# Kernel optimization log

Hardware: AMD Instinct MI355X
Metric: run time of the kernel (lower is better)

## Reference

```python
import jax, jax.numpy as jnp
import numpy as np

RADIUS, HMIN, HMAX, NSAMPLE = 0.05, -0.02, 0.04, 32
EPS = 1e-5


def setup_inputs() -> dict:
    key = jax.random.key(0)
    ks = jax.random.split(key, 6)
    B, N, C, OUT = 4, 2048, 256, 256
    seed_xyz_graspable = jax.random.uniform(ks[0], (B, N, 3), jnp.float32) * 0.2
    seed_features_graspable = jax.random.normal(ks[1], (B, C, N), jnp.float32)
    vp_rot = jax.random.normal(ks[2], (B, N, 3, 3), jnp.float32)
    W1 = jax.random.normal(ks[3], (OUT, 3 + C), jnp.float32) * 0.02
    W2 = jax.random.normal(ks[4], (OUT, OUT), jnp.float32) * 0.02
    return {
        "seed_xyz_graspable": seed_xyz_graspable,
        "seed_features_graspable": seed_features_graspable,
        "vp_rot": vp_rot,
        "W1": W1, "gamma1": jnp.ones((OUT,), jnp.float32), "beta1": jnp.zeros((OUT,), jnp.float32),
        "W2": W2, "gamma2": jnp.ones((OUT,), jnp.float32), "beta2": jnp.zeros((OUT,), jnp.float32),
    }


def _cylinder_query(xyz, rot):
    # xyz: (B,N,3), rot: (B,N,3,3); new_xyz == xyz.
    B, N, _ = xyz.shape
    d = xyz[:, None, :, :] - xyz[:, :, None, :]                  # (B,P,N,3) offsets to each candidate
    r = jnp.einsum('bpij,bpnj->bpni', rot, d)                    # rotate into cylinder frame (rot @ d)
    mask = (r[..., 1] ** 2 + r[..., 2] ** 2 < RADIUS ** 2) & (r[..., 0] > HMIN) & (r[..., 0] < HMAX)
    order = jnp.arange(N, dtype=jnp.int32)
    keys = jnp.where(mask, order, order + N)                     # in-cylinder points sort first, stable order
    _, idx = jax.lax.top_k(-keys, NSAMPLE)                       # first NSAMPLE indices satisfying the query
    valid = jnp.take_along_axis(mask, idx, axis=-1)
    first = idx[..., :1]
    any_valid = valid[..., :1]
    idx = jnp.where(valid, idx, jnp.where(any_valid, first, 0))  # pad with first hit like the CUDA kernel
    return idx                                                   # (B,P,NSAMPLE) int32


def _group(xyz, features, rot, idx):
    gxyz = jax.vmap(lambda a, i: a[i])(xyz, idx)                 # (B,P,S,3)
    gxyz = (gxyz - xyz[:, :, None, :]) / RADIUS                  # center on query + normalize_xyz
    gxyz = jnp.einsum('bpsj,bpjk->bpsk', gxyz, rot)              # rotate_xyz: grouped_xyz @ rot
    gfeat = jax.vmap(lambda f, i: f[:, i])(features, idx)        # (B,C,P,S)
    return jnp.concatenate([gxyz.transpose(0, 3, 1, 2), gfeat], axis=1)  # (B,3+C,P,S)


def _conv_bn_relu(x, W, gamma, beta):
    y = jnp.einsum('oc,bcps->bops', W, x)                        # 1x1 conv, no bias (bn=True)
    mu = y.mean(axis=(0, 2, 3), keepdims=True)
    var = y.var(axis=(0, 2, 3), keepdims=True)
    y = (y - mu) * jax.lax.rsqrt(var + EPS)
    y = y * gamma[None, :, None, None] + beta[None, :, None, None]
    return jax.nn.relu(y)


def reference(seed_xyz_graspable, seed_features_graspable, vp_rot, W1, gamma1, beta1, W2, gamma2, beta2):
    idx = _cylinder_query(seed_xyz_graspable, vp_rot)
    g = _group(seed_xyz_graspable, seed_features_graspable, vp_rot, idx)
    h = _conv_bn_relu(g, W1, gamma1, beta1)
    h = _conv_bn_relu(h, W2, gamma2, beta2)
    return h.max(axis=3)                                         # maxpool over nsample -> (B,OUT,P)
```

## Files before the change

kernel.cpp:

```cpp
#include <hip/hip_runtime.h>

typedef unsigned short u16;
typedef unsigned int u32;
typedef __attribute__((ext_vector_type(8))) short bf16x8;
typedef __attribute__((ext_vector_type(4))) float f32x4;

#define NPTS 2048
#define CFEAT 256
#define NS 32
#define MTOT 262144
#define NBLK 4096
#define INV_N (1.0f/262144.0f)

__device__ __forceinline__ float bf2f(u16 u) {
    union { u32 i; float f; } v; v.i = ((u32)u) << 16; return v.f;
}
__device__ __forceinline__ u16 f2bf(float f) {
    union { float f; u32 i; } v; v.f = f;
    u32 i = v.i;
    return (u16)((i + 0x7fffu + ((i >> 16) & 1u)) >> 16);
}

__device__ __forceinline__ void gload16(const void* g, void* l) {
    __builtin_amdgcn_global_load_lds((const __attribute__((address_space(1))) void*)g,
                                     (__attribute__((address_space(3))) void*)l, 16, 0, 0);
}

__global__ __launch_bounds__(256) void prep_k(const float* __restrict__ W1, const float* __restrict__ W2,
                                              u16* __restrict__ Wp1, u16* __restrict__ Wp2) {
    int o = blockIdx.x, t = threadIdx.x;
    Wp1[o * 288 + t] = f2bf(W1[o * 259 + 3 + t]);
    if (t < 32) Wp1[o * 288 + 256 + t] = (t < 3) ? f2bf(W1[o * 259 + t]) : (u16)0;
    Wp2[o * 256 + t] = f2bf(W2[o * 256 + t]);
}

__global__ __launch_bounds__(256) void query_k(const float* __restrict__ xyz, const float* __restrict__ rot,
                                               int* __restrict__ idx) {
    int pid = blockIdx.x * 4 + (threadIdx.x >> 6);
    int lane = threadIdx.x & 63;
    int b = pid >> 11, p = pid & 2047;
    const float* xb = xyz + (size_t)b * NPTS * 3;
    float px = xb[p * 3 + 0], py = xb[p * 3 + 1], pz = xb[p * 3 + 2];
    const float* rp = rot + (size_t)pid * 9;
    float r00 = rp[0], r01 = rp[1], r02 = rp[2];
    float r10 = rp[3], r11 = rp[4], r12 = rp[5];
    float r20 = rp[6], r21 = rp[7], r22 = rp[8];
    int cnt = 0, first = 0;
    for (int n0 = 0; n0 < NPTS && cnt < NS; n0 += 64) {
        int n = n0 + lane;
        float dx = __fsub_rn(xb[n * 3 + 0], px);
        float dy = __fsub_rn(xb[n * 3 + 1], py);
        float dz = __fsub_rn(xb[n * 3 + 2], pz);
        float a0 = __fadd_rn(__fadd_rn(__fmul_rn(r00, dx), __fmul_rn(r01, dy)), __fmul_rn(r02, dz));
        float a1 = __fadd_rn(__fadd_rn(__fmul_rn(r10, dx), __fmul_rn(r11, dy)), __fmul_rn(r12, dz));
        float a2 = __fadd_rn(__fadd_rn(__fmul_rn(r20, dx), __fmul_rn(r21, dy)), __fmul_rn(r22, dz));
        float t2 = __fadd_rn(__fmul_rn(a1, a1), __fmul_rn(a2, a2));
        bool valid = (t2 < 0.0025f) && (a0 > -0.02f) && (a0 < 0.04f);
        unsigned long long bal = __ballot(valid);
        if (cnt == 0 && bal) first = n0 + __builtin_ctzll(bal);
        int rank = __builtin_popcountll(bal & ((1ull << lane) - 1ull));
        int slot = cnt + rank;
        if (valid && slot < NS) idx[(size_t)pid * NS + slot] = n;
        cnt += __builtin_popcountll(bal);
    }
    int filled = cnt < NS ? cnt : NS;
    if (lane >= filled && lane < NS) idx[(size_t)pid * NS + lane] = (cnt > 0) ? first : 0;
}

__global__ __launch_bounds__(256) void featT_k(const float* __restrict__ feat, u16* __restrict__ featT) {
    __shared__ float sm[32 * 33];
    int b = blockIdx.z;
    int n0 = blockIdx.x * 32, c0 = blockIdx.y * 32;
    int t = threadIdx.x, x = t & 31, y = t >> 5;
    #pragma unroll
    for (int rr = 0; rr < 4; rr++) {
        int c = c0 + y + rr * 8;
        sm[(y + rr * 8) * 33 + x] = feat[((size_t)(b * CFEAT + c)) * NPTS + n0 + x];
    }
    __syncthreads();
    #pragma unroll
    for (int rr = 0; rr < 4; rr++) {
        int n = n0 + y + rr * 8;
        featT[((size_t)(b * NPTS + n)) * CFEAT + c0 + x] = f2bf(sm[x * 33 + (y + rr * 8)]);
    }
}

__global__ __launch_bounds__(256) void gxyz_k(const float* __restrict__ xyz, const float* __restrict__ rot,
                                              const int* __restrict__ idx, u16* __restrict__ gxyz) {
    int m = blockIdx.x * 256 + threadIdx.x;
    int pid = m >> 5;
    int b = pid >> 11, p = pid & 2047;
    int i = idx[m];
    const float* xb = xyz + (size_t)b * NPTS * 3;
    float dx = (xb[i * 3 + 0] - xb[p * 3 + 0]) * 20.0f;
    float dy = (xb[i * 3 + 1] - xb[p * 3 + 1]) * 20.0f;
    float dz = (xb[i * 3 + 2] - xb[p * 3 + 2]) * 20.0f;
    const float* rp = rot + (size_t)pid * 9;
    float g0 = dx * rp[0] + dy * rp[3] + dz * rp[6];
    float g1 = dx * rp[1] + dy * rp[4] + dz * rp[7];
    float g2 = dx * rp[2] + dy * rp[5] + dz * rp[8];
    uint2 v;
    v.x = (u32)f2bf(g0) | ((u32)f2bf(g1) << 16);
    v.y = (u32)f2bf(g2);
    *(uint2*)(gxyz + (size_t)m * 4) = v;
}

template <int FULL, int STORE>
__global__ __launch_bounds__(256) void fused_k(
    const u16* __restrict__ featT, const u16* __restrict__ gxyz, const int* __restrict__ idx,
    const u16* __restrict__ Wp1, const u16* __restrict__ Wp2, const float* __restrict__ ab1,
    float* __restrict__ psum, float* __restrict__ psq,
    float* __restrict__ ymax, float* __restrict__ ymin, uint2* __restrict__ y1f)
{
    __shared__ __attribute__((aligned(16))) u16 As[64 * 32];
    __shared__ __attribute__((aligned(16))) u16 Bs[256 * 32];
    __shared__ __attribute__((aligned(16))) u16 y1s[FULL ? 64 * 264 : 16];
    __shared__ int rowbase_s[64];

    const int tid = threadIdx.x;
    const int lane = tid & 63, wave = tid >> 6;
    const int quad = lane >> 4, tl = lane & 15;
    const int bx = blockIdx.x;
    const int m0 = bx * 64;

    if (tid < 64) {
        int m = m0 + tid;
        int gi = idx[m];
        int b = m >> 16;
        rowbase_s[tid] = (b * NPTS + gi) * CFEAT;
    }
    __syncthreads();
    const int srow = tid >> 2, sc16 = tid & 3;
    const int abase = rowbase_s[srow] + sc16 * 8;

    f32x4 acc[4][4];
    #pragma unroll
    for (int i = 0; i < 4; i++)
        #pragma unroll
        for (int j = 0; j < 4; j++) acc[i][j] = (f32x4){0.f, 0.f, 0.f, 0.f};

    auto mfma_tile = [&](f32x4 (&ac)[4][4], const u16* a_lds, int a_stride) {
        bf16x8 af[4], bv[4];
        #pragma unroll
        for (int i = 0; i < 4; i++) af[i] = *(const bf16x8*)(a_lds + (i * 16 + tl) * a_stride + quad * 8);
        #pragma unroll
        for (int j = 0; j < 4; j++) bv[j] = *(const bf16x8*)(Bs + (wave * 64 + j * 16 + tl) * 32 + quad * 8);
        #pragma unroll
        for (int i = 0; i < 4; i++)
            #pragma unroll
            for (int j = 0; j < 4; j++)
                ac[i][j] = __builtin_amdgcn_mfma_f32_16x16x32_bf16(af[i], bv[j], ac[i][j], 0, 0, 0);
    };

    for (int ks = 0; ks < 8; ks++) {
        const int k0 = ks * 32;
        __syncthreads();
        gload16(featT + abase + k0, As + tid * 8);
        #pragma unroll
        for (int q = 0; q < 4; q++)
            gload16(Wp1 + (srow + q * 64) * 288 + k0 + sc16 * 8, Bs + q * 2048 + tid * 8);
        __syncthreads();
        mfma_tile(acc, As, 32);
    }
    {
        __syncthreads();
        uint4 va = make_uint4(0, 0, 0, 0);
        if (sc16 == 0) {
            uint2 g2 = *(const uint2*)(gxyz + (size_t)(m0 + srow) * 4);
            va.x = g2.x; va.y = g2.y;
        }
        *(uint4*)(As + srow * 32 + sc16 * 8) = va;
        #pragma unroll
        for (int q = 0; q < 4; q++)
            gload16(Wp1 + (srow + q * 64) * 288 + 256 + sc16 * 8, Bs + q * 2048 + tid * 8);
        __syncthreads();
        mfma_tile(acc, As, 32);
    }

    if (!FULL) {
        #pragma unroll
        for (int j = 0; j < 4; j++) {
            float s = 0.f, q2 = 0.f;
            #pragma unroll
            for (int i = 0; i < 4; i++) {
                float v0 = acc[i][j][0], v1 = acc[i][j][1], v2 = acc[i][j][2], v3 = acc[i][j][3];
                if (STORE) {
                    u32 lo = (u32)f2bf(v0) | ((u32)f2bf(v1) << 16);
                    u32 hi = (u32)f2bf(v2) | ((u32)f2bf(v3) << 16);
                    y1f[((size_t)(bx * 4 + wave) * 16 + i * 4 + j) * 64 + lane] = make_uint2(lo, hi);
                    v0 = bf2f((u16)(lo & 0xffff)); v1 = bf2f((u16)(lo >> 16));
                    v2 = bf2f((u16)(hi & 0xffff)); v3 = bf2f((u16)(hi >> 16));
                }
                s += v0 + v1 + v2 + v3;
                q2 += v0 * v0 + v1 * v1 + v2 * v2 + v3 * v3;
            }
            s += __shfl_xor(s, 16); s += __shfl_xor(s, 32);
            q2 += __shfl_xor(q2, 16); q2 += __shfl_xor(q2, 32);
            if (quad == 0) {
                int col = wave * 64 + j * 16 + tl;
                psum[(size_t)bx * 256 + col] = s;
                psq[(size_t)bx * 256 + col] = q2;
            }
        }
        return;
    }

    #pragma unroll
    for (int j = 0; j < 4; j++) {
        int col = wave * 64 + j * 16 + tl;
        float a = ab1[col], bb = ab1[256 + col];
        #pragma unroll
        for (int i = 0; i < 4; i++)
            #pragma unroll
            for (int r = 0; r < 4; r++) {
                float v = fmaxf(fmaf(acc[i][j][r], a, bb), 0.f);
                y1s[(i * 16 + quad * 4 + r) * 264 + col] = f2bf(v);
            }
    }

    f32x4 acc2[4][4];
    #pragma unroll
    for (int i = 0; i < 4; i++)
        #pragma unroll
        for (int j = 0; j < 4; j++) acc2[i][j] = (f32x4){0.f, 0.f, 0.f, 0.f};
    for (int ks = 0; ks < 8; ks++) {
        const int k0 = ks * 32;
        __syncthreads();
        #pragma unroll
        for (int q = 0; q < 4; q++)
            gload16(Wp2 + (srow + q * 64) * 256 + k0 + sc16 * 8, Bs + q * 2048 + tid * 8);
        __syncthreads();
        mfma_tile(acc2, y1s + k0, 264);
    }

    #pragma unroll
    for (int j = 0; j < 4; j++) {
        int col = wave * 64 + j * 16 + tl;
        float s = 0.f, q2 = 0.f;
        float mx0 = -3.0e38f, mn0 = 3.0e38f, mx1 = -3.0e38f, mn1 = 3.0e38f;
        #pragma unroll
        for (int i = 0; i < 4; i++)
            #pragma unroll
            for (int r = 0; r < 4; r++) {
                float v = acc2[i][j][r];
                s += v; q2 += v * v;
                if (i < 2) { mx0 = fmaxf(mx0, v); mn0 = fminf(mn0, v); }
                else       { mx1 = fmaxf(mx1, v); mn1 = fminf(mn1, v); }
            }
        s += __shfl_xor(s, 16); s += __shfl_xor(s, 32);
        q2 += __shfl_xor(q2, 16); q2 += __shfl_xor(q2, 32);
        mx0 = fmaxf(mx0, __shfl_xor(mx0, 16)); mx0 = fmaxf(mx0, __shfl_xor(mx0, 32));
        mn0 = fminf(mn0, __shfl_xor(mn0, 16)); mn0 = fminf(mn0, __shfl_xor(mn0, 32));
        mx1 = fmaxf(mx1, __shfl_xor(mx1, 16)); mx1 = fmaxf(mx1, __shfl_xor(mx1, 32));
        mn1 = fminf(mn1, __shfl_xor(mn1, 16)); mn1 = fminf(mn1, __shfl_xor(mn1, 32));
        if (quad == 0) {
            psum[(size_t)bx * 256 + col] = s;
            psq[(size_t)bx * 256 + col] = q2;
            size_t p0 = (size_t)(bx * 2) * 256 + col;
            size_t p1 = (size_t)(bx * 2 + 1) * 256 + col;
            ymax[p0] = mx0; ymin[p0] = mn0;
            ymax[p1] = mx1; ymin[p1] = mn1;
        }
    }
}

__global__ __launch_bounds__(256) void fused2_k(
    const uint2* __restrict__ y1f, const u16* __restrict__ Wp2, const float* __restrict__ ab1,
    float* __restrict__ psum, float* __restrict__ psq,
    float* __restrict__ ymax, float* __restrict__ ymin)
{
    __shared__ __attribute__((aligned(16))) u16 Bs[256 * 32];
    __shared__ __attribute__((aligned(16))) u16 y1s[64 * 264];
    const int tid = threadIdx.x;
    const int lane = tid & 63, wave = tid >> 6;
    const int quad = lane >> 4, tl = lane & 15;
    const int bx = blockIdx.x;

    #pragma unroll
    for (int j = 0; j < 4; j++) {
        int col = wave * 64 + j * 16 + tl;
        float a = ab1[col], bb = ab1[256 + col];
        #pragma unroll
        for (int i = 0; i < 4; i++) {
            uint2 v = y1f[((size_t)(bx * 4 + wave) * 16 + i * 4 + j) * 64 + lane];
            float f0 = bf2f((u16)(v.x & 0xffff)), f1 = bf2f((u16)(v.x >> 16));
            float f2 = bf2f((u16)(v.y & 0xffff)), f3 = bf2f((u16)(v.y >> 16));
            int rb = (i * 16 + quad * 4) * 264 + col;
            y1s[rb] = f2bf(fmaxf(fmaf(f0, a, bb), 0.f));
            y1s[rb + 264] = f2bf(fmaxf(fmaf(f1, a, bb), 0.f));
            y1s[rb + 528] = f2bf(fmaxf(fmaf(f2, a, bb), 0.f));
            y1s[rb + 792] = f2bf(fmaxf(fmaf(f3, a, bb), 0.f));
        }
    }

    const int srow = tid >> 2, sc16 = tid & 3;
    f32x4 acc2[4][4];
    #pragma unroll
    for (int i = 0; i < 4; i++)
        #pragma unroll
        for (int j = 0; j < 4; j++) acc2[i][j] = (f32x4){0.f, 0.f, 0.f, 0.f};

    for (int ks = 0; ks < 8; ks++) {
        const int k0 = ks * 32;
        __syncthreads();
        #pragma unroll
        for (int q = 0; q < 4; q++)
            gload16(Wp2 + (srow + q * 64) * 256 + k0 + sc16 * 8, Bs + q * 2048 + tid * 8);
        __syncthreads();
        bf16x8 af[4], bv[4];
        #pragma unroll
        for (int i = 0; i < 4; i++) af[i] = *(const bf16x8*)(y1s + (i * 16 + tl) * 264 + k0 + quad * 8);
        #pragma unroll
        for (int j = 0; j < 4; j++) bv[j] = *(const bf16x8*)(Bs + (wave * 64 + j * 16 + tl) * 32 + quad * 8);
        #pragma unroll
        for (int i = 0; i < 4; i++)
            #pragma unroll
            for (int j = 0; j < 4; j++)
                acc2[i][j] = __builtin_amdgcn_mfma_f32_16x16x32_bf16(af[i], bv[j], acc2[i][j], 0, 0, 0);
    }

    #pragma unroll
    for (int j = 0; j < 4; j++) {
        int col = wave * 64 + j * 16 + tl;
        float s = 0.f, q2 = 0.f;
        float mx0 = -3.0e38f, mn0 = 3.0e38f, mx1 = -3.0e38f, mn1 = 3.0e38f;
        #pragma unroll
        for (int i = 0; i < 4; i++)
            #pragma unroll
            for (int r = 0; r < 4; r++) {
                float v = acc2[i][j][r];
                s += v; q2 += v * v;
                if (i < 2) { mx0 = fmaxf(mx0, v); mn0 = fminf(mn0, v); }
                else       { mx1 = fmaxf(mx1, v); mn1 = fminf(mn1, v); }
            }
        s += __shfl_xor(s, 16); s += __shfl_xor(s, 32);
        q2 += __shfl_xor(q2, 16); q2 += __shfl_xor(q2, 32);
        mx0 = fmaxf(mx0, __shfl_xor(mx0, 16)); mx0 = fmaxf(mx0, __shfl_xor(mx0, 32));
        mn0 = fminf(mn0, __shfl_xor(mn0, 16)); mn0 = fminf(mn0, __shfl_xor(mn0, 32));
        mx1 = fmaxf(mx1, __shfl_xor(mx1, 16)); mx1 = fmaxf(mx1, __shfl_xor(mx1, 32));
        mn1 = fminf(mn1, __shfl_xor(mn1, 16)); mn1 = fminf(mn1, __shfl_xor(mn1, 32));
        if (quad == 0) {
            psum[(size_t)bx * 256 + col] = s;
            psq[(size_t)bx * 256 + col] = q2;
            size_t p0 = (size_t)(bx * 2) * 256 + col;
            size_t p1 = (size_t)(bx * 2 + 1) * 256 + col;
            ymax[p0] = mx0; ymin[p0] = mn0;
            ymax[p1] = mx1; ymin[p1] = mn1;
        }
    }
}

__global__ __launch_bounds__(256) void reduce1_k(const float* __restrict__ psum, const float* __restrict__ psq,
                                                 float* __restrict__ ps2, float* __restrict__ pq2) {
    int j = blockIdx.x, t = threadIdx.x;
    float s = 0.f, q = 0.f;
    #pragma unroll 4
    for (int kk = 0; kk < 16; kk++) {
        size_t r = (size_t)(j * 16 + kk) * 256 + t;
        s += psum[r]; q += psq[r];
    }
    ps2[j * 256 + t] = s;
    pq2[j * 256 + t] = q;
}

__global__ __launch_bounds__(256) void reduce2_k(const float* __restrict__ ps2, const float* __restrict__ pq2,
                                                 const float* __restrict__ gamma, const float* __restrict__ beta,
                                                 float* __restrict__ ab) {
    int c = threadIdx.x;
    float S = 0.f, Q = 0.f;
    for (int j = 0; j < 256; j++) {
        S += ps2[j * 256 + c];
        Q += pq2[j * 256 + c];
    }
    float mu = S * INV_N;
    float var = Q * INV_N - mu * mu;
    float a = gamma[c] * rsqrtf(var + 1e-5f);
    ab[c] = a;
    ab[256 + c] = beta[c] - mu * a;
}

__global__ __launch_bounds__(256) void final_k(const float* __restrict__ ymax, const float* __restrict__ ymin,
                                               const float* __restrict__ ab, float* __restrict__ out) {
    __shared__ float sm[32 * 33];
    int b = blockIdx.z;
    int n0 = blockIdx.x * 32, o0 = blockIdx.y * 32;
    int t = threadIdx.x, x = t & 31, y = t >> 5;
    #pragma unroll
    for (int rr = 0; rr < 4; rr++) {
        int n = n0 + y + rr * 8;
        int o = o0 + x;
        float a = ab[o], bb = ab[256 + o];
        size_t p = (size_t)(b * NPTS + n) * 256 + o;
        float v = (a >= 0.f) ? ymax[p] : ymin[p];
        sm[(y + rr * 8) * 33 + x] = fmaxf(fmaf(v, a, bb), 0.f);
    }
    __syncthreads();
    #pragma unroll
    for (int rr = 0; rr < 4; rr++)
        out[((size_t)(b * 256 + o0 + y + rr * 8)) * NPTS + n0 + x] = sm[x * 33 + (y + rr * 8)];
}

extern "C" void kernel_launch(void* const* d_in, const int* in_sizes, int n_in,
                              void* d_out, int out_size, void* d_ws, size_t ws_size,
                              hipStream_t stream) {
    const float* xyz    = (const float*)d_in[0];
    const float* feat   = (const float*)d_in[1];
    const float* rot    = (const float*)d_in[2];
    const float* W1     = (const float*)d_in[3];
    const float* gamma1 = (const float*)d_in[4];
    const float* beta1  = (const float*)d_in[5];
    const float* W2     = (const float*)d_in[6];
    const float* gamma2 = (const float*)d_in[7];
    const float* beta2  = (const float*)d_in[8];
    float* out = (float*)d_out;

    char* ws = (char*)d_ws;
    u16*   featT = (u16*)(ws + 0);
    int*   idx   = (int*)(ws + 4194304);
    u16*   gxyz  = (u16*)(ws + 5242880);
    u16*   Wp1   = (u16*)(ws + 7340032);
    u16*   Wp2   = (u16*)(ws + 7487488);
    float* ab1   = (float*)(ws + 7618560);
    float* ab2   = (float*)(ws + 7620608);
    float* psum  = (float*)(ws + 7622656);
    float* psq   = (float*)(ws + 11816960);
    float* ymax  = (float*)(ws + 16011264);
    float* ymin  = (float*)(ws + 24399872);
    uint2* y1f   = (uint2*)(ws + 32788480);
    const size_t BIG_NEED = 32788480ull + 134217728ull;

    float* r1s = (float*)(ws + 24399872);
    float* r1q = r1s + 65536;
    float* r2s = (float*)(ws + 5242880);
    float* r2q = r2s + 65536;

    prep_k<<<256, 256, 0, stream>>>(W1, W2, Wp1, Wp2);
    query_k<<<2048, 256, 0, stream>>>(xyz, rot, idx);
    featT_k<<<dim3(64, 8, 4), 256, 0, stream>>>(feat, featT);
    gxyz_k<<<1024, 256, 0, stream>>>(xyz, rot, idx, gxyz);

    if (ws_size >= BIG_NEED) {
        fused_k<0, 1><<<NBLK, 256, 0, stream>>>(featT, gxyz, idx, Wp1, Wp2, ab1, psum, psq, ymax, ymin, y1f);
        reduce1_k<<<256, 256, 0, stream>>>(psum, psq, r1s, r1q);
        reduce2_k<<<1, 256, 0, stream>>>(r1s, r1q, gamma1, beta1, ab1);
        fused2_k<<<NBLK, 256, 0, stream>>>(y1f, Wp2, ab1, psum, psq, ymax, ymin);
        reduce1_k<<<256, 256, 0, stream>>>(psum, psq, r2s, r2q);
        reduce2_k<<<1, 256, 0, stream>>>(r2s, r2q, gamma2, beta2, ab2);
    } else {
        fused_k<0, 0><<<NBLK, 256, 0, stream>>>(featT, gxyz, idx, Wp1, Wp2, ab1, psum, psq, ymax, ymin, nullptr);
        reduce1_k<<<256, 256, 0, stream>>>(psum, psq, r1s, r1q);
        reduce2_k<<<1, 256, 0, stream>>>(r1s, r1q, gamma1, beta1, ab1);
        fused_k<1, 0><<<NBLK, 256, 0, stream>>>(featT, gxyz, idx, Wp1, Wp2, ab1, psum, psq, ymax, ymin, nullptr);
        reduce1_k<<<256, 256, 0, stream>>>(psum, psq, r2s, r2q);
        reduce2_k<<<1, 256, 0, stream>>>(r2s, r2q, gamma2, beta2, ab2);
    }
    final_k<<<dim3(64, 8, 4), 256, 0, stream>>>(ymax, ymin, ab2, out);
}
```

Before: 258.2 us.

## Compute BN1 statistics from per-point GEMM weighted by gather counts

Layer-1 batch-norm statistics are no longer computed over the full gathered 262144-row GEMM. They come from a GEMM over only the 8192 unique points, weighted by how often each point is gathered, plus closed-form terms for the xyz channels (counts via atomics, second moments of gxyz). This removes the separate first-pass GEMM and the large bf16 intermediate buffer. The full kernel also double-buffers its LDS tiles to overlap global loads with MFMA. The trade-offs are atomic contention in count_k and a small change in numerics, since statistics now come from fp32 accumulators rather than bf16-rounded values.

```diff
diff --git a/kernel.cpp b/kernel.cpp
--- a/kernel.cpp
+++ b/kernel.cpp
@@ -10,6 +10,7 @@
 #define NS 32
 #define MTOT 262144
 #define NBLK 4096
+#define NROW 8192
 #define INV_N (1.0f/262144.0f)
 
 __device__ __forceinline__ float bf2f(u16 u) {
@@ -105,16 +106,141 @@
     *(uint2*)(gxyz + (size_t)m * 4) = v;
 }
 
-template <int FULL, int STORE>
-__global__ __launch_bounds__(256) void fused_k(
+__global__ __launch_bounds__(256) void zero_k(float* __restrict__ p, int n) {
+    int i = blockIdx.x * 256 + threadIdx.x;
+    if (i < n) p[i] = 0.f;
+}
+
+__global__ __launch_bounds__(256) void count_k(const int* __restrict__ idx, const u16* __restrict__ gxyz,
+                                               float* __restrict__ cntx, float* __restrict__ xstat) {
+    __shared__ float red[9 * 4];
+    int t = threadIdx.x, lane = t & 63, wave = t >> 6;
+    float p[9] = {0.f,0.f,0.f,0.f,0.f,0.f,0.f,0.f,0.f};
+    #pragma unroll
+    for (int u = 0; u < 4; u++) {
+        int m = blockIdx.x * 1024 + u * 256 + t;
+        int b = m >> 16;
+        int r = (b << 11) + idx[m];
+        uint2 v = *(const uint2*)(gxyz + (size_t)m * 4);
+        float x0 = bf2f((u16)(v.x & 0xffff));
+        float x1 = bf2f((u16)(v.x >> 16));
+        float x2 = bf2f((u16)(v.y & 0xffff));
+        atomicAdd(cntx + r * 4 + 0, 1.f);
+        atomicAdd(cntx + r * 4 + 1, x0);
+        atomicAdd(cntx + r * 4 + 2, x1);
+        atomicAdd(cntx + r * 4 + 3, x2);
+        p[0] += x0; p[1] += x1; p[2] += x2;
+        p[3] += x0 * x0; p[4] += x0 * x1; p[5] += x0 * x2;
+        p[6] += x1 * x1; p[7] += x1 * x2; p[8] += x2 * x2;
+    }
+    #pragma unroll
+    for (int k = 0; k < 9; k++) {
+        float s = p[k];
+        #pragma unroll
+        for (int o = 1; o < 64; o <<= 1) s += __shfl_xor(s, o);
+        if (lane == 0) red[k * 4 + wave] = s;
+    }
+    __syncthreads();
+    if (t < 9) atomicAdd(xstat + t, red[t * 4 + 0] + red[t * 4 + 1] + red[t * 4 + 2] + red[t * 4 + 3]);
+}
+
+__global__ __launch_bounds__(256) void zgemm_k(const u16* __restrict__ featT, const u16* __restrict__ Wp1,
+                                               const float* __restrict__ cntx,
+                                               float* __restrict__ Sacc, float* __restrict__ Qacc,
+                                               float* __restrict__ Xacc) {
+    __shared__ __attribute__((aligned(16))) u16 As[64 * 32];
+    __shared__ __attribute__((aligned(16))) u16 Bs[256 * 32];
+    const int tid = threadIdx.x;
+    const int lane = tid & 63, wave = tid >> 6;
+    const int quad = lane >> 4, tl = lane & 15;
+    const int m0 = blockIdx.x * 64;
+    const int srow = tid >> 2, sc16 = tid & 3;
+    const int abase = (m0 + srow) * CFEAT + sc16 * 8;
+
+    f32x4 acc[4][4];
+    #pragma unroll
+    for (int i = 0; i < 4; i++)
+        #pragma unroll
+        for (int j = 0; j < 4; j++) acc[i][j] = (f32x4){0.f, 0.f, 0.f, 0.f};
+
+    for (int ks = 0; ks < 8; ks++) {
+        const int k0 = ks * 32;
+        __syncthreads();
+        gload16(featT + abase + k0, As + tid * 8);
+        #pragma unroll
+        for (int q = 0; q < 4; q++)
+            gload16(Wp1 + (srow + q * 64) * 288 + k0 + sc16 * 8, Bs + q * 2048 + tid * 8);
+        __syncthreads();
+        bf16x8 af[4], bv[4];
+        #pragma unroll
+        for (int i = 0; i < 4; i++) af[i] = *(const bf16x8*)(As + (i * 16 + tl) * 32 + quad * 8);
+        #pragma unroll
+        for (int j = 0; j < 4; j++) bv[j] = *(const bf16x8*)(Bs + (wave * 64 + j * 16 + tl) * 32 + quad * 8);
+        #pragma unroll
+        for (int i = 0; i < 4; i++)
+            #pragma unroll
+            for (int j = 0; j < 4; j++)
+                acc[i][j] = __builtin_amdgcn_mfma_f32_16x16x32_bf16(af[i], bv[j], acc[i][j], 0, 0, 0);
+    }
+
+    #pragma unroll
+    for (int j = 0; j < 4; j++) {
+        int col = wave * 64 + j * 16 + tl;
+        float wx0 = bf2f(Wp1[col * 288 + 256]);
+        float wx1 = bf2f(Wp1[col * 288 + 257]);
+        float wx2 = bf2f(Wp1[col * 288 + 258]);
+        float S = 0.f, Q = 0.f, X = 0.f;
+        #pragma unroll
+        for (int i = 0; i < 4; i++)
+            #pragma unroll
+            for (int rr = 0; rr < 4; rr++) {
+                int row = i * 16 + quad * 4 + rr;
+                float4 cx = *(const float4*)(cntx + (size_t)(m0 + row) * 4);
+                float z = acc[i][j][rr];
+                S += cx.x * z;
+                Q += cx.x * z * z;
+                X += z * (wx0 * cx.y + wx1 * cx.z + wx2 * cx.w);
+            }
+        S += __shfl_xor(S, 16); S += __shfl_xor(S, 32);
+        Q += __shfl_xor(Q, 16); Q += __shfl_xor(Q, 32);
+        X += __shfl_xor(X, 16); X += __shfl_xor(X, 32);
+        if (quad == 0) {
+            atomicAdd(Sacc + col, S);
+            atomicAdd(Qacc + col, Q);
+            atomicAdd(Xacc + col, X);
+        }
+    }
+}
+
+__global__ __launch_bounds__(256) void ab1_k(const float* __restrict__ Sacc, const float* __restrict__ Qacc,
+                                             const float* __restrict__ Xacc, const float* __restrict__ xstat,
+                                             const u16* __restrict__ Wp1,
+                                             const float* __restrict__ gamma, const float* __restrict__ beta,
+                                             float* __restrict__ ab) {
+    int c = threadIdx.x;
+    float wx0 = bf2f(Wp1[c * 288 + 256]);
+    float wx1 = bf2f(Wp1[c * 288 + 257]);
+    float wx2 = bf2f(Wp1[c * 288 + 258]);
+    float S = Sacc[c] + wx0 * xstat[0] + wx1 * xstat[1] + wx2 * xstat[2];
+    float qxx = wx0 * wx0 * xstat[3] + wx1 * wx1 * xstat[6] + wx2 * wx2 * xstat[8]
+              + 2.f * (wx0 * wx1 * xstat[4] + wx0 * wx2 * xstat[5] + wx1 * wx2 * xstat[7]);
+    float Q = Qacc[c] + 2.f * Xacc[c] + qxx;
+    float mu = S * INV_N;
+    float var = Q * INV_N - mu * mu;
+    float a = gamma[c] * rsqrtf(var + 1e-5f);
+    ab[c] = a;
+    ab[256 + c] = beta[c] - mu * a;
+}
+
+__global__ __launch_bounds__(256) void full_k(
     const u16* __restrict__ featT, const u16* __restrict__ gxyz, const int* __restrict__ idx,
     const u16* __restrict__ Wp1, const u16* __restrict__ Wp2, const float* __restrict__ ab1,
     float* __restrict__ psum, float* __restrict__ psq,
-    float* __restrict__ ymax, float* __restrict__ ymin, uint2* __restrict__ y1f)
+    float* __restrict__ ymax, float* __restrict__ ymin)
 {
-    __shared__ __attribute__((aligned(16))) u16 As[64 * 32];
-    __shared__ __attribute__((aligned(16))) u16 Bs[256 * 32];
-    __shared__ __attribute__((aligned(16))) u16 y1s[FULL ? 64 * 264 : 16];
+    __shared__ __attribute__((aligned(16))) u16 As[2][64 * 32];
+    __shared__ __attribute__((aligned(16))) u16 Bs[2][256 * 32];
+    __shared__ __attribute__((aligned(16))) u16 y1s[64 * 264];
     __shared__ int rowbase_s[64];
 
     const int tid = threadIdx.x;
@@ -133,18 +259,12 @@
     const int srow = tid >> 2, sc16 = tid & 3;
     const int abase = rowbase_s[srow] + sc16 * 8;
 
-    f32x4 acc[4][4];
-    #pragma unroll
-    for (int i = 0; i < 4; i++)
-        #pragma unroll
-        for (int j = 0; j < 4; j++) acc[i][j] = (f32x4){0.f, 0.f, 0.f, 0.f};
-
-    auto mfma_tile = [&](f32x4 (&ac)[4][4], const u16* a_lds, int a_stride) {
+    auto mfma_tile = [&](f32x4 (&ac)[4][4], const u16* a_lds, int a_stride, const u16* b_lds) {
         bf16x8 af[4], bv[4];
         #pragma unroll
         for (int i = 0; i < 4; i++) af[i] = *(const bf16x8*)(a_lds + (i * 16 + tl) * a_stride + quad * 8);
         #pragma unroll
-        for (int j = 0; j < 4; j++) bv[j] = *(const bf16x8*)(Bs + (wave * 64 + j * 16 + tl) * 32 + quad * 8);
+        for (int j = 0; j < 4; j++) bv[j] = *(const bf16x8*)(b_lds + (wave * 64 + j * 16 + tl) * 32 + quad * 8);
         #pragma unroll
         for (int i = 0; i < 4; i++)
             #pragma unroll
@@ -152,57 +272,38 @@
                 ac[i][j] = __builtin_amdgcn_mfma_f32_16x16x32_bf16(af[i], bv[j], ac[i][j], 0, 0, 0);
     };
 
-    for (int ks = 0; ks < 8; ks++) {
-        const int k0 = ks * 32;
-        __syncthreads();
-        gload16(featT + abase + k0, As + tid * 8);
-        #pragma unroll
-        for (int q = 0; q < 4; q++)
-            gload16(Wp1 + (srow + q * 64) * 288 + k0 + sc16 * 8, Bs + q * 2048 + tid * 8);
-        __syncthreads();
-        mfma_tile(acc, As, 32);
-    }
-    {
-        __syncthreads();
-        uint4 va = make_uint4(0, 0, 0, 0);
-        if (sc16 == 0) {
-            uint2 g2 = *(const uint2*)(gxyz + (size_t)(m0 + srow) * 4);
-            va.x = g2.x; va.y = g2.y;
+    auto stage1 = [&](int t, int buf) {
+        if (t < 8) {
+            gload16(featT + abase + t * 32, &As[buf][tid * 8]);
+            #pragma unroll
+            for (int q = 0; q < 4; q++)
+                gload16(Wp1 + (srow + q * 64) * 288 + t * 32 + sc16 * 8, &Bs[buf][q * 2048 + tid * 8]);
+        } else {
+            uint4 va = make_uint4(0, 0, 0, 0);
+            if (sc16 == 0) {
+                uint2 g2 = *(const uint2*)(gxyz + (size_t)(m0 + srow) * 4);
+                va.x = g2.x; va.y = g2.y;
+            }
+            *(uint4*)(&As[buf][srow * 32 + sc16 * 8]) = va;
+            #pragma unroll
+            for (int q = 0; q < 4; q++)
+                gload16(Wp1 + (srow + q * 64) * 288 + 256 + sc16 * 8, &Bs[buf][q * 2048 + tid * 8]);
         }
-        *(uint4*)(As + srow * 32 + sc16 * 8) = va;
-        #pragma unroll
-        for (int q = 0; q < 4; q++)
-            gload16(Wp1 + (srow + q * 64) * 288 + 256 + sc16 * 8, Bs + q * 2048 + tid * 8);
-        __syncthreads();
-        mfma_tile(acc, As, 32);
-    }
-
-    if (!FULL) {
-        #pragma unroll
-        for (int j = 0; j < 4; j++) {
-            float s = 0.f, q2 = 0.f;
-            #pragma unroll
-            for (int i = 0; i < 4; i++) {
-                float v0 = acc[i][j][0], v1 = acc[i][j][1], v2 = acc[i][j][2], v3 = acc[i][j][3];
-                if (STORE) {
-                    u32 lo = (u32)f2bf(v0) | ((u32)f2bf(v1) << 16);
-                    u32 hi = (u32)f2bf(v2) | ((u32)f2bf(v3) << 16);
-                    y1f[((size_t)(bx * 4 + wave) * 16 + i * 4 + j) * 64 + lane] = make_uint2(lo, hi);
-                    v0 = bf2f((u16)(lo & 0xffff)); v1 = bf2f((u16)(lo >> 16));
-                    v2 = bf2f((u16)(hi & 0xffff)); v3 = bf2f((u16)(hi >> 16));
-                }
-                s += v0 + v1 + v2 + v3;
-                q2 += v0 * v0 + v1 * v1 + v2 * v2 + v3 * v3;
-            }
-            s += __shfl_xor(s, 16); s += __shfl_xor(s, 32);
-            q2 += __shfl_xor(q2, 16); q2 += __shfl_xor(q2, 32);
-            if (quad == 0) {
-                int col = wave * 64 + j * 16 + tl;
-                psum[(size_t)bx * 256 + col] = s;
-                psq[(size_t)bx * 256 + col] = q2;
-            }
-        }
-        return;
+    };
+
+    f32x4 acc[4][4];
+    #pragma unroll
+    for (int i = 0; i < 4; i++)
+        #pragma unroll
+        for (int j = 0; j < 4; j++) acc[i][j] = (f32x4){0.f, 0.f, 0.f, 0.f};
+
+    stage1(0, 0);
+    __syncthreads();
+    for (int t = 0; t < 9; t++) {
+        const int cur = t & 1;
+        if (t < 8) stage1(t + 1, cur ^ 1);
+        mfma_tile(acc, &As[cur][0], 32, &Bs[cur][0]);
+        __syncthreads();
     }
 
     #pragma unroll
@@ -217,20 +318,25 @@
                 y1s[(i * 16 + quad * 4 + r) * 264 + col] = f2bf(v);
             }
     }
+    #pragma unroll
+    for (int q = 0; q < 4; q++)
+        gload16(Wp2 + (srow + q * 64) * 256 + sc16 * 8, &Bs[0][q * 2048 + tid * 8]);
+    __syncthreads();
 
     f32x4 acc2[4][4];
     #pragma unroll
     for (int i = 0; i < 4; i++)
         #pragma unroll
         for (int j = 0; j < 4; j++) acc2[i][j] = (f32x4){0.f, 0.f, 0.f, 0.f};
-    for (int ks = 0; ks < 8; ks++) {
-        const int k0 = ks * 32;
-        __syncthreads();
-        #pragma unroll
-        for (int q = 0; q < 4; q++)
-            gload16(Wp2 + (srow + q * 64) * 256 + k0 + sc16 * 8, Bs + q * 2048 + tid * 8);
-        __syncthreads();
-        mfma_tile(acc2, y1s + k0, 264);
+    for (int t = 0; t < 8; t++) {
+        const int cur = t & 1;
+        if (t < 7) {
+            #pragma unroll
+            for (int q = 0; q < 4; q++)
+                gload16(Wp2 + (srow + q * 64) * 256 + (t + 1) * 32 + sc16 * 8, &Bs[cur ^ 1][q * 2048 + tid * 8]);
+        }
+        mfma_tile(acc2, y1s + t * 32, 264, &Bs[cur][0]);
+        __syncthreads();
     }
 
     #pragma unroll
@@ -264,42 +370,117 @@
     }
 }
 
-__global__ __launch_bounds__(256) void fused2_k(
-    const uint2* __restrict__ y1f, const u16* __restrict__ Wp2, const float* __restrict__ ab1,
+template <int FULL>
+__global__ __launch_bounds__(256) void fused_k(
+    const u16* __restrict__ featT, const u16* __restrict__ gxyz, const int* __restrict__ idx,
+    const u16* __restrict__ Wp1, const u16* __restrict__ Wp2, const float* __restrict__ ab1,
     float* __restrict__ psum, float* __restrict__ psq,
     float* __restrict__ ymax, float* __restrict__ ymin)
 {
+    __shared__ __attribute__((aligned(16))) u16 As[64 * 32];
     __shared__ __attribute__((aligned(16))) u16 Bs[256 * 32];
-    __shared__ __attribute__((aligned(16))) u16 y1s[64 * 264];
+    __shared__ __attribute__((aligned(16))) u16 y1s[FULL ? 64 * 264 : 16];
+    __shared__ int rowbase_s[64];
+
     const int tid = threadIdx.x;
     const int lane = tid & 63, wave = tid >> 6;
     const int quad = lane >> 4, tl = lane & 15;
     const int bx = blockIdx.x;
+    const int m0 = bx * 64;
+
+    if (tid < 64) {
+        int m = m0 + tid;
+        int gi = idx[m];
+        int b = m >> 16;
+        rowbase_s[tid] = (b * NPTS + gi) * CFEAT;
+    }
+    __syncthreads();
+    const int srow = tid >> 2, sc16 = tid & 3;
+    const int abase = rowbase_s[srow] + sc16 * 8;
+
+    f32x4 acc[4][4];
+    #pragma unroll
+    for (int i = 0; i < 4; i++)
+        #pragma unroll
+        for (int j = 0; j < 4; j++) acc[i][j] = (f32x4){0.f, 0.f, 0.f, 0.f};
+
+    auto mfma_tile = [&](f32x4 (&ac)[4][4], const u16* a_lds, int a_stride) {
+        bf16x8 af[4], bv[4];
+        #pragma unroll
+        for (int i = 0; i < 4; i++) af[i] = *(const bf16x8*)(a_lds + (i * 16 + tl) * a_stride + quad * 8);
+        #pragma unroll
+        for (int j = 0; j < 4; j++) bv[j] = *(const bf16x8*)(Bs + (wave * 64 + j * 16 + tl) * 32 + quad * 8);
+        #pragma unroll
+        for (int i = 0; i < 4; i++)
+            #pragma unroll
+            for (int j = 0; j < 4; j++)
+                ac[i][j] = __builtin_amdgcn_mfma_f32_16x16x32_bf16(af[i], bv[j], ac[i][j], 0, 0, 0);
+    };
+
+    for (int ks = 0; ks < 8; ks++) {
+        const int k0 = ks * 32;
+        __syncthreads();
+        gload16(featT + abase + k0, As + tid * 8);
+        #pragma unroll
+        for (int q = 0; q < 4; q++)
+            gload16(Wp1 + (srow + q * 64) * 288 + k0 + sc16 * 8, Bs + q * 2048 + tid * 8);
+        __syncthreads();
+        mfma_tile(acc, As, 32);
+    }
+    {
+        __syncthreads();
+        uint4 va = make_uint4(0, 0, 0, 0);
+        if (sc16 == 0) {
+            uint2 g2 = *(const uint2*)(gxyz + (size_t)(m0 + srow) * 4);
+            va.x = g2.x; va.y = g2.y;
+        }
+        *(uint4*)(As + srow * 32 + sc16 * 8) = va;
+        #pragma unroll
+        for (int q = 0; q < 4; q++)
+            gload16(Wp1 + (srow + q * 64) * 288 + 256 + sc16 * 8, Bs + q * 2048 + tid * 8);
+        __syncthreads();
+        mfma_tile(acc, As, 32);
+    }
+
+    if (!FULL) {
+        #pragma unroll
+        for (int j = 0; j < 4; j++) {
+            float s = 0.f, q2 = 0.f;
+            #pragma unroll
+            for (int i = 0; i < 4; i++) {
+                s += acc[i][j][0] + acc[i][j][1] + acc[i][j][2] + acc[i][j][3];
+                q2 += acc[i][j][0]*acc[i][j][0] + acc[i][j][1]*acc[i][j][1]
+                    + acc[i][j][2]*acc[i][j][2] + acc[i][j][3]*acc[i][j][3];
+            }
+            s += __shfl_xor(s, 16); s += __shfl_xor(s, 32);
+            q2 += __shfl_xor(q2, 16); q2 += __shfl_xor(q2, 32);
+            if (quad == 0) {
+                int col = wave * 64 + j * 16 + tl;
+                psum[(size_t)bx * 256 + col] = s;
+                psq[(size_t)bx * 256 + col] = q2;
+            }
+        }
+        return;
+    }
 
     #pragma unroll
     for (int j = 0; j < 4; j++) {
         int col = wave * 64 + j * 16 + tl;
         float a = ab1[col], bb = ab1[256 + col];
         #pragma unroll
-        for (int i = 0; i < 4; i++) {
-            uint2 v = y1f[((size_t)(bx * 4 + wave) * 16 + i * 4 + j) * 64 + lane];
-            float f0 = bf2f((u16)(v.x & 0xffff)), f1 = bf2f((u16)(v.x >> 16));
-            float f2 = bf2f((u16)(v.y & 0xffff)), f3 = bf2f((u16)(v.y >> 16));
-            int rb = (i * 16 + quad * 4) * 264 + col;
-            y1s[rb] = f2bf(fmaxf(fmaf(f0, a, bb), 0.f));
-            y1s[rb + 264] = f2bf(fmaxf(fmaf(f1, a, bb), 0.f));
-            y1s[rb + 528] = f2bf(fmaxf(fmaf(f2, a, bb), 0.f));
-            y1s[rb + 792] = f2bf(fmaxf(fmaf(f3, a, bb), 0.f));
-        }
-    }
-
-    const int srow = tid >> 2, sc16 = tid & 3;
+        for (int i = 0; i < 4; i++)
+            #pragma unroll
+            for (int r = 0; r < 4; r++) {
+                float v = fmaxf(fmaf(acc[i][j][r], a, bb), 0.f);
+                y1s[(i * 16 + quad * 4 + r) * 264 + col] = f2bf(v);
+            }
+    }
+
     f32x4 acc2[4][4];
     #pragma unroll
     for (int i = 0; i < 4; i++)
         #pragma unroll
         for (int j = 0; j < 4; j++) acc2[i][j] = (f32x4){0.f, 0.f, 0.f, 0.f};
-
     for (int ks = 0; ks < 8; ks++) {
         const int k0 = ks * 32;
         __syncthreads();
@@ -307,16 +488,7 @@
         for (int q = 0; q < 4; q++)
             gload16(Wp2 + (srow + q * 64) * 256 + k0 + sc16 * 8, Bs + q * 2048 + tid * 8);
         __syncthreads();
-        bf16x8 af[4], bv[4];
-        #pragma unroll
-        for (int i = 0; i < 4; i++) af[i] = *(const bf16x8*)(y1s + (i * 16 + tl) * 264 + k0 + quad * 8);
-        #pragma unroll
-        for (int j = 0; j < 4; j++) bv[j] = *(const bf16x8*)(Bs + (wave * 64 + j * 16 + tl) * 32 + quad * 8);
-        #pragma unroll
-        for (int i = 0; i < 4; i++)
-            #pragma unroll
-            for (int j = 0; j < 4; j++)
-                acc2[i][j] = __builtin_amdgcn_mfma_f32_16x16x32_bf16(af[i], bv[j], acc2[i][j], 0, 0, 0);
+        mfma_tile(acc2, y1s + k0, 264);
     }
 
     #pragma unroll
@@ -355,8 +527,8 @@
     int j = blockIdx.x, t = threadIdx.x;
     float s = 0.f, q = 0.f;
     #pragma unroll 4
-    for (int kk = 0; kk < 16; kk++) {
-        size_t r = (size_t)(j * 16 + kk) * 256 + t;
+    for (int kk = 0; kk < 64; kk++) {
+        size_t r = (size_t)(j * 64 + kk) * 256 + t;
         s += psum[r]; q += psq[r];
     }
     ps2[j * 256 + t] = s;
@@ -368,7 +540,7 @@
                                                  float* __restrict__ ab) {
     int c = threadIdx.x;
     float S = 0.f, Q = 0.f;
-    for (int j = 0; j < 256; j++) {
+    for (int j = 0; j < 64; j++) {
         S += ps2[j * 256 + c];
         Q += pq2[j * 256 + c];
     }
@@ -416,42 +588,49 @@
 
     char* ws = (char*)d_ws;
     u16*   featT = (u16*)(ws + 0);
-    int*   idx   = (int*)(ws + 4194304);
+    int*   idxp  = (int*)(ws + 4194304);
     u16*   gxyz  = (u16*)(ws + 5242880);
     u16*   Wp1   = (u16*)(ws + 7340032);
     u16*   Wp2   = (u16*)(ws + 7487488);
     float* ab1   = (float*)(ws + 7618560);
     float* ab2   = (float*)(ws + 7620608);
-    float* psum  = (float*)(ws + 7622656);
-    float* psq   = (float*)(ws + 11816960);
-    float* ymax  = (float*)(ws + 16011264);
-    float* ymin  = (float*)(ws + 24399872);
-    uint2* y1f   = (uint2*)(ws + 32788480);
-    const size_t BIG_NEED = 32788480ull + 134217728ull;
-
-    float* r1s = (float*)(ws + 24399872);
-    float* r1q = r1s + 65536;
+    float* sb    = (float*)(ws + 7622656);
+    float* psum  = (float*)(ws + 7756928);
+    float* psq   = (float*)(ws + 11951232);
+    float* ymax  = (float*)(ws + 16145536);
+    float* ymin  = (float*)(ws + 24534144);
+    const size_t NEED = 32922752ull;
+
+    float* cntx = sb;
+    float* Sacc = sb + 32768;
+    float* Qacc = sb + 33024;
+    float* Xacc = sb + 33280;
+    float* xst  = sb + 33536;
+
+    float* r1s = (float*)(ws + 24534144);
+    float* r1q = r1s + 16384;
     float* r2s = (float*)(ws + 5242880);
-    float* r2q = r2s + 65536;
+    float* r2q = r2s + 16384;
 
     prep_k<<<256, 256, 0, stream>>>(W1, W2, Wp1, Wp2);
-    query_k<<<2048, 256, 0, stream>>>(xyz, rot, idx);
+    query_k<<<2048, 256, 0, stream>>>(xyz, rot, idxp);
     featT_k<<<dim3(64, 8, 4), 256, 0, stream>>>(feat, featT);
-    gxyz_k<<<1024, 256, 0, stream>>>(xyz, rot, idx, gxyz);
-
-    if (ws_size >= BIG_NEED) {
-        fused_k<0, 1><<<NBLK, 256, 0, stream>>>(featT, gxyz, idx, Wp1, Wp2, ab1, psum, psq, ymax, ymin, y1f);
-        reduce1_k<<<256, 256, 0, stream>>>(psum, psq, r1s, r1q);
-        reduce2_k<<<1, 256, 0, stream>>>(r1s, r1q, gamma1, beta1, ab1);
-        fused2_k<<<NBLK, 256, 0, stream>>>(y1f, Wp2, ab1, psum, psq, ymax, ymin);
-        reduce1_k<<<256, 256, 0, stream>>>(psum, psq, r2s, r2q);
+    gxyz_k<<<1024, 256, 0, stream>>>(xyz, rot, idxp, gxyz);
+
+    if (ws_size >= NEED) {
+        zero_k<<<132, 256, 0, stream>>>(sb, 33552);
+        count_k<<<256, 256, 0, stream>>>(idxp, gxyz, cntx, xst);
+        zgemm_k<<<NROW / 64, 256, 0, stream>>>(featT, Wp1, cntx, Sacc, Qacc, Xacc);
+        ab1_k<<<1, 256, 0, stream>>>(Sacc, Qacc, Xacc, xst, Wp1, gamma1, beta1, ab1);
+        full_k<<<NBLK, 256, 0, stream>>>(featT, gxyz, idxp, Wp1, Wp2, ab1, psum, psq, ymax, ymin);
+        reduce1_k<<<64, 256, 0, stream>>>(psum, psq, r2s, r2q);
         reduce2_k<<<1, 256, 0, stream>>>(r2s, r2q, gamma2, beta2, ab2);
     } else {
-        fused_k<0, 0><<<NBLK, 256, 0, stream>>>(featT, gxyz, idx, Wp1, Wp2, ab1, psum, psq, ymax, ymin, nullptr);
-        reduce1_k<<<256, 256, 0, stream>>>(psum, psq, r1s, r1q);
+        fused_k<0><<<NBLK, 256, 0, stream>>>(featT, gxyz, idxp, Wp1, Wp2, ab1, psum, psq, ymax, ymin);
+        reduce1_k<<<64, 256, 0, stream>>>(psum, psq, r1s, r1q);
         reduce2_k<<<1, 256, 0, stream>>>(r1s, r1q, gamma1, beta1, ab1);
-        fused_k<1, 0><<<NBLK, 256, 0, stream>>>(featT, gxyz, idx, Wp1, Wp2, ab1, psum, psq, ymax, ymin, nullptr);
-        reduce1_k<<<256, 256, 0, stream>>>(psum, psq, r2s, r2q);
+        fused_k<1><<<NBLK, 256, 0, stream>>>(featT, gxyz, idxp, Wp1, Wp2, ab1, psum, psq, ymax, ymin);
+        reduce1_k<<<64, 256, 0, stream>>>(psum, psq, r2s, r2q);
         reduce2_k<<<1, 256, 0, stream>>>(r2s, r2q, gamma2, beta2, ab2);
     }
     final_k<<<dim3(64, 8, 4), 256, 0, stream>>>(ymax, ymin, ab2, out);
```

Result: slower. 415.5 us (+60.9%).
